# Kernel tuning notes

Measured on AMD Instinct MI355X. Metric: run time of the kernel, lower is better.

## Reference

```python
import jax, jax.numpy as jnp
import numpy as np

B, L, D, H = 4, 256, 256, 8
DH = D // H


def setup_inputs() -> dict:
    key = jax.random.key(0)
    ks = jax.random.split(key, 12)
    s = 1.0 / np.sqrt(D)
    return {
        "inputs": jax.random.normal(ks[0], (B, L, D), jnp.float32),
        "mask": jax.random.bernoulli(ks[1], 0.15, (B, L, L)),
        "rel_emb": jax.random.normal(ks[2], (B, L, L, D), jnp.float32) * 0.05,
        "Wq": jax.random.normal(ks[3], (D, D), jnp.float32) * s,
        "bq": jnp.zeros((D,), jnp.float32),
        "Wk": jax.random.normal(ks[4], (D, D), jnp.float32) * s,
        "bk": jnp.zeros((D,), jnp.float32),
        "Wv": jax.random.normal(ks[5], (D, D), jnp.float32) * s,
        "bv": jnp.zeros((D,), jnp.float32),
        "Wo": jax.random.normal(ks[6], (D, D), jnp.float32) * s,
        "bo": jnp.zeros((D,), jnp.float32),
        "u": jax.random.normal(ks[7], (D,), jnp.float32),
        "v_param": jax.random.normal(ks[8], (D,), jnp.float32),
    }


def _shape(x):
    # (B, L, D) -> (B, H, L, DH)
    return x.reshape(B, L, H, DH).transpose(0, 2, 1, 3)


def reference(inputs, mask, rel_emb, Wq, bq, Wk, bk, Wv, bv, Wo, bo, u, v_param):
    q = _shape(inputs @ Wq.T + bq) / np.sqrt(DH)  # (B,H,L,DH), pre-scaled
    k = _shape(inputs @ Wk.T + bk)
    val = _shape(inputs @ Wv.T + bv)

    u_h = u.reshape(1, H, 1, DH)
    v_h = v_param.reshape(1, H, 1, DH)

    # content term: (q+u) k^T
    a_c = jnp.einsum('bhqd,bhkd->bhqk', q + u_h, k)
    # position term: (q+v) rel_emb^T, rel_emb per (q,k) pair
    rel = rel_emb.reshape(B, L, L, H, DH)
    b_d = jnp.einsum('bhqd,bqkhd->bhqk', q + v_h, rel)

    scores = (a_c + b_d).astype(jnp.float32)
    scores = jnp.where(mask[:, None, :, :], -1e18, scores)
    attn = jax.nn.softmax(scores, axis=-1)  # (B,H,L,L)

    ctx = jnp.einsum('bhqk,bhkd->bhqd', attn, val)
    ctx = ctx.transpose(0, 2, 1, 3).reshape(B, L, D)
    out = ctx @ Wo.T + bo
    return (out, attn)
```

## Files before the change

### kernel.cpp

```cpp
#include <hip/hip_runtime.h>
#include <hip/hip_bf16.h>

#define BB  4
#define LL  256
#define DD  256
#define HH  8
#define DHH 32
#define BL  1024

__global__ __launch_bounds__(1024) void mask_detect_kernel(
    const unsigned int* __restrict__ w, unsigned int* __restrict__ flags) {
  __shared__ int sf32, shib;
  const int t = threadIdx.x;
  if (t == 0) { sf32 = 0; shib = 0; }
  __syncthreads();
  int f = 0, hb = 0;
  for (int i = t; i < 16384; i += 1024) {
    unsigned int x = w[i];
    if (x == 0x3F800000u) f = 1;
    else if (x & 0xFFFFFF00u) hb = 1;
  }
  if (f)  atomicOr(&sf32, 1);
  if (hb) atomicOr(&shib, 1);
  __syncthreads();
  if (t == 0) flags[0] = (sf32 || !shib) ? 1u : 0u;
}

__global__ __launch_bounds__(256) void qkv_kernel(
    const float* __restrict__ X,
    const float* __restrict__ Wq, const float* __restrict__ bq,
    const float* __restrict__ Wk, const float* __restrict__ bk,
    const float* __restrict__ Wv, const float* __restrict__ bv,
    const float* __restrict__ u,  const float* __restrict__ vp,
    float* __restrict__ qu, float* __restrict__ qv,
    float* __restrict__ K,  float* __restrict__ V) {
  const int row0 = blockIdx.x * 4;
  const int c = threadIdx.x;
  float accq[4] = {0.f, 0.f, 0.f, 0.f};
  float acck[4] = {0.f, 0.f, 0.f, 0.f};
  float accv[4] = {0.f, 0.f, 0.f, 0.f};
  const float4* Wq4 = (const float4*)(Wq + c * DD);
  const float4* Wk4 = (const float4*)(Wk + c * DD);
  const float4* Wv4 = (const float4*)(Wv + c * DD);
  const float4* X4  = (const float4*)X;
  const int xbase = row0 * (DD / 4);
#pragma unroll 8
  for (int j4 = 0; j4 < DD / 4; ++j4) {
    const float4 wq = Wq4[j4], wk = Wk4[j4], wv = Wv4[j4];
#pragma unroll
    for (int r = 0; r < 4; ++r) {
      const float4 x = X4[xbase + r * (DD / 4) + j4];
      accq[r] += x.x * wq.x + x.y * wq.y + x.z * wq.z + x.w * wq.w;
      acck[r] += x.x * wk.x + x.y * wk.y + x.z * wk.z + x.w * wk.w;
      accv[r] += x.x * wv.x + x.y * wv.y + x.z * wv.z + x.w * wv.w;
    }
  }
  const float scale = 0.17677669529663687f;
  const float uc = u[c], vc = vp[c], bqc = bq[c], bkc = bk[c], bvc = bv[c];
#pragma unroll
  for (int r = 0; r < 4; ++r) {
    const int idx = (row0 + r) * DD + c;
    const float pq = (accq[r] + bqc) * scale;
    qu[idx] = pq + uc;
    qv[idx] = pq + vc;
    K[idx]  = acck[r] + bkc;
    V[idx]  = accv[r] + bvc;
  }
}

__global__ __launch_bounds__(256) void attn_kernel(
    const float* __restrict__ qu, const float* __restrict__ qv,
    const float* __restrict__ Km, const float* __restrict__ Vm,
    const float* __restrict__ rel, const void* __restrict__ mask_raw,
    const unsigned int* __restrict__ flags,
    float* __restrict__ attn_out, float* __restrict__ ctx) {
  const int bq = blockIdx.x;
  const int b = bq >> 8, q = bq & 255;
  const int t = threadIdx.x;
  const int wave = t >> 6, lane = t & 63;
  __shared__ float qu_s[DD], qv_s[DD];
  __shared__ float msk_s[LL];
  __shared__ float sc[HH][LL + 4];

  qu_s[t] = qu[bq * DD + t];
  qv_s[t] = qv[bq * DD + t];
  bool masked;
  if (flags[0]) masked = ((const unsigned int*)mask_raw)[bq * LL + t] != 0u;
  else          masked = ((const unsigned char*)mask_raw)[bq * LL + t] != 0;
  msk_s[t] = masked ? 1.f : 0.f;
  __syncthreads();

  const float4 u4 = ((const float4*)qu_s)[lane];
  const float4 w4 = ((const float4*)qv_s)[lane];
  const int h_of_lane = lane >> 3;
  const float4* K4 = (const float4*)(Km + (size_t)b * LL * DD) +
                     (size_t)(wave * 64) * 64 + lane;
  const float4* R4 = (const float4*)(rel + (size_t)bq * LL * DD) +
                     (size_t)(wave * 64) * 64 + lane;
#pragma unroll 4
  for (int i = 0; i < 64; ++i) {
    const int k = wave * 64 + i;
    const float4 kk = K4[(size_t)i * 64];
    const float4 rr = R4[(size_t)i * 64];
    float s = u4.x * kk.x + u4.y * kk.y + u4.z * kk.z + u4.w * kk.w
            + w4.x * rr.x + w4.y * rr.y + w4.z * rr.z + w4.w * rr.w;
    s += __shfl_xor(s, 1);
    s += __shfl_xor(s, 2);
    s += __shfl_xor(s, 4);
    if ((lane & 7) == 0)
      sc[h_of_lane][k] = (msk_s[k] != 0.f) ? -1e18f : s;
  }
  __syncthreads();

#pragma unroll
  for (int hh = 0; hh < 2; ++hh) {
    const int h = wave * 2 + hh;
    float v0 = sc[h][lane], v1 = sc[h][lane + 64];
    float v2 = sc[h][lane + 128], v3 = sc[h][lane + 192];
    float m = fmaxf(fmaxf(v0, v1), fmaxf(v2, v3));
#pragma unroll
    for (int off = 32; off >= 1; off >>= 1) m = fmaxf(m, __shfl_xor(m, off));
    float e0 = __expf(v0 - m), e1 = __expf(v1 - m);
    float e2 = __expf(v2 - m), e3 = __expf(v3 - m);
    float s = (e0 + e1) + (e2 + e3);
#pragma unroll
    for (int off = 32; off >= 1; off >>= 1) s += __shfl_xor(s, off);
    const float inv = 1.0f / s;
    e0 *= inv; e1 *= inv; e2 *= inv; e3 *= inv;
    sc[h][lane] = e0; sc[h][lane + 64] = e1;
    sc[h][lane + 128] = e2; sc[h][lane + 192] = e3;
    float* aout = attn_out + (((size_t)(b * HH + h) * LL + q) * LL);
    aout[lane] = e0; aout[lane + 64] = e1;
    aout[lane + 128] = e2; aout[lane + 192] = e3;
  }
  __syncthreads();

  const int h = t >> 5;
  const float* Vb = Vm + (size_t)b * LL * DD + t;
  float c0 = 0.f, c1 = 0.f, c2 = 0.f, c3 = 0.f;
#pragma unroll 4
  for (int k = 0; k < LL; k += 4) {
    c0 += sc[h][k + 0] * Vb[(size_t)(k + 0) * DD];
    c1 += sc[h][k + 1] * Vb[(size_t)(k + 1) * DD];
    c2 += sc[h][k + 2] * Vb[(size_t)(k + 2) * DD];
    c3 += sc[h][k + 3] * Vb[(size_t)(k + 3) * DD];
  }
  ctx[bq * DD + t] = (c0 + c1) + (c2 + c3);
}

__global__ __launch_bounds__(256) void outproj_kernel(
    const float* __restrict__ ctx, const float* __restrict__ Wo,
    const float* __restrict__ bo, float* __restrict__ out) {
  const int row0 = blockIdx.x * 4;
  const int c = threadIdx.x;
  float acc[4] = {0.f, 0.f, 0.f, 0.f};
  const float4* W4 = (const float4*)(Wo + c * DD);
  const float4* X4 = (const float4*)ctx;
  const int xbase = row0 * (DD / 4);
#pragma unroll 8
  for (int j4 = 0; j4 < DD / 4; ++j4) {
    const float4 w = W4[j4];
#pragma unroll
    for (int r = 0; r < 4; ++r) {
      const float4 x = X4[xbase + r * (DD / 4) + j4];
      acc[r] += x.x * w.x + x.y * w.y + x.z * w.z + x.w * w.w;
    }
  }
  const float boc = bo[c];
#pragma unroll
  for (int r = 0; r < 4; ++r) out[(row0 + r) * DD + c] = acc[r] + boc;
}

extern "C" void kernel_launch(void* const* d_in, const int* in_sizes, int n_in,
                              void* d_out, int out_size, void* d_ws, size_t ws_size,
                              hipStream_t stream) {
  (void)in_sizes; (void)n_in; (void)out_size; (void)ws_size;
  const float* X   = (const float*)d_in[0];
  const void*  msk = d_in[1];
  const float* rel = (const float*)d_in[2];
  const float* Wq  = (const float*)d_in[3];
  const float* bq  = (const float*)d_in[4];
  const float* Wk  = (const float*)d_in[5];
  const float* bk  = (const float*)d_in[6];
  const float* Wv  = (const float*)d_in[7];
  const float* bv  = (const float*)d_in[8];
  const float* Wo  = (const float*)d_in[9];
  const float* bo  = (const float*)d_in[10];
  const float* u   = (const float*)d_in[11];
  const float* vp  = (const float*)d_in[12];

  float* out  = (float*)d_out;
  float* attn = out + BL * DD;

  float* ws_f = (float*)d_ws;
  float* qu  = ws_f;
  float* qv  = qu + BL * DD;
  float* K   = qv + BL * DD;
  float* V   = K  + BL * DD;
  float* ctx = V  + BL * DD;
  unsigned int* flags = (unsigned int*)(ctx + BL * DD);

  mask_detect_kernel<<<1, 1024, 0, stream>>>((const unsigned int*)msk, flags);
  qkv_kernel<<<BL / 4, 256, 0, stream>>>(X, Wq, bq, Wk, bk, Wv, bv, u, vp,
                                         qu, qv, K, V);
  attn_kernel<<<BL, 256, 0, stream>>>(qu, qv, K, V, rel, msk, flags, attn, ctx);
  outproj_kernel<<<BL / 4, 256, 0, stream>>>(ctx, Wo, bo, out);
}
```

Baseline: 111.0 us.

## Use 512-thread attention blocks with per-wave key split and shared ctx reduction

The attention kernel now runs 8 waves per block instead of 4. Each wave handles 32 keys for the score pass, one head for the softmax, and a 32-key slice of the P·V product. The P·V product switches from strided scalar V loads to coalesced float4 loads, writes partial context vectors to shared memory, and reduces them at the end. The aim is more memory-level parallelism on the dominant rel_emb stream and better V access, at the cost of an extra shared buffer, another barrier and a reduction step.

```diff
diff --git a/kernel.cpp b/kernel.cpp
--- a/kernel.cpp
+++ b/kernel.cpp
@@ -68,7 +68,7 @@
   }
 }
 
-__global__ __launch_bounds__(256) void attn_kernel(
+__global__ __launch_bounds__(512, 8) void attn_kernel(
     const float* __restrict__ qu, const float* __restrict__ qv,
     const float* __restrict__ Km, const float* __restrict__ Vm,
     const float* __restrict__ rel, const void* __restrict__ mask_raw,
@@ -81,25 +81,29 @@
   __shared__ float qu_s[DD], qv_s[DD];
   __shared__ float msk_s[LL];
   __shared__ float sc[HH][LL + 4];
-
-  qu_s[t] = qu[bq * DD + t];
-  qv_s[t] = qv[bq * DD + t];
-  bool masked;
-  if (flags[0]) masked = ((const unsigned int*)mask_raw)[bq * LL + t] != 0u;
-  else          masked = ((const unsigned char*)mask_raw)[bq * LL + t] != 0;
-  msk_s[t] = masked ? 1.f : 0.f;
+  __shared__ float pctx[HH][DD + 4];
+
+  if (t < 256) {
+    qu_s[t] = qu[bq * DD + t];
+    qv_s[t] = qv[bq * DD + t];
+    bool masked;
+    if (flags[0]) masked = ((const unsigned int*)mask_raw)[bq * LL + t] != 0u;
+    else          masked = ((const unsigned char*)mask_raw)[bq * LL + t] != 0;
+    msk_s[t] = masked ? 1.f : 0.f;
+  }
   __syncthreads();
 
   const float4 u4 = ((const float4*)qu_s)[lane];
   const float4 w4 = ((const float4*)qv_s)[lane];
   const int h_of_lane = lane >> 3;
+  const int k0 = wave * 32;
   const float4* K4 = (const float4*)(Km + (size_t)b * LL * DD) +
-                     (size_t)(wave * 64) * 64 + lane;
+                     (size_t)k0 * 64 + lane;
   const float4* R4 = (const float4*)(rel + (size_t)bq * LL * DD) +
-                     (size_t)(wave * 64) * 64 + lane;
+                     (size_t)k0 * 64 + lane;
 #pragma unroll 4
-  for (int i = 0; i < 64; ++i) {
-    const int k = wave * 64 + i;
+  for (int i = 0; i < 32; ++i) {
+    const int k = k0 + i;
     const float4 kk = K4[(size_t)i * 64];
     const float4 rr = R4[(size_t)i * 64];
     float s = u4.x * kk.x + u4.y * kk.y + u4.z * kk.z + u4.w * kk.w
@@ -112,9 +116,8 @@
   }
   __syncthreads();
 
-#pragma unroll
-  for (int hh = 0; hh < 2; ++hh) {
-    const int h = wave * 2 + hh;
+  {
+    const int h = wave;
     float v0 = sc[h][lane], v1 = sc[h][lane + 64];
     float v2 = sc[h][lane + 128], v3 = sc[h][lane + 192];
     float m = fmaxf(fmaxf(v0, v1), fmaxf(v2, v3));
@@ -135,17 +138,27 @@
   }
   __syncthreads();
 
-  const int h = t >> 5;
-  const float* Vb = Vm + (size_t)b * LL * DD + t;
-  float c0 = 0.f, c1 = 0.f, c2 = 0.f, c3 = 0.f;
+  {
+    const float4* V4 = (const float4*)(Vm + (size_t)b * LL * DD) +
+                       (size_t)k0 * 64 + lane;
+    float4 acc = make_float4(0.f, 0.f, 0.f, 0.f);
 #pragma unroll 4
-  for (int k = 0; k < LL; k += 4) {
-    c0 += sc[h][k + 0] * Vb[(size_t)(k + 0) * DD];
-    c1 += sc[h][k + 1] * Vb[(size_t)(k + 1) * DD];
-    c2 += sc[h][k + 2] * Vb[(size_t)(k + 2) * DD];
-    c3 += sc[h][k + 3] * Vb[(size_t)(k + 3) * DD];
-  }
-  ctx[bq * DD + t] = (c0 + c1) + (c2 + c3);
+    for (int i = 0; i < 32; ++i) {
+      const float a = sc[h_of_lane][k0 + i];
+      const float4 vv = V4[(size_t)i * 64];
+      acc.x += a * vv.x; acc.y += a * vv.y;
+      acc.z += a * vv.z; acc.w += a * vv.w;
+    }
+    ((float4*)&pctx[wave][0])[lane] = acc;
+  }
+  __syncthreads();
+
+  if (t < 256) {
+    float s = 0.f;
+#pragma unroll
+    for (int w = 0; w < HH; ++w) s += pctx[w][t];
+    ctx[bq * DD + t] = s;
+  }
 }
 
 __global__ __launch_bounds__(256) void outproj_kernel(
@@ -203,6 +216,6 @@
   mask_detect_kernel<<<1, 1024, 0, stream>>>((const unsigned int*)msk, flags);
   qkv_kernel<<<BL / 4, 256, 0, stream>>>(X, Wq, bq, Wk, bk, Wv, bv, u, vp,
                                          qu, qv, K, V);
-  attn_kernel<<<BL, 256, 0, stream>>>(qu, qv, K, V, rel, msk, flags, attn, ctx);
+  attn_kernel<<<BL, 512, 0, stream>>>(qu, qv, K, V, rel, msk, flags, attn, ctx);
   outproj_kernel<<<BL / 4, 256, 0, stream>>>(ctx, Wo, bo, out);
 }
```

Measured after the change: 113.1 us. No clear change (+1.9%).
